# Optimization experiments

Hardware: AMD Instinct MI355X
Metric: run time of the kernel (lower is better)

The kernel has to match this reference:

```python
import jax, jax.numpy as jnp
import numpy as np

EPS = 1e-12  # F.normalize eps

def _l2norm(v, axis):
    n = jnp.sqrt(jnp.sum(v * v, axis=axis, keepdims=True))
    return v / jnp.maximum(n, EPS)

def setup_inputs() -> dict:
    key = jax.random.key(0)
    k1, k2, k3, k4 = jax.random.split(key, 4)
    B, N, D, K = 32, 8192, 128, 64
    x = jax.random.normal(k1, (B, N, D), dtype=jnp.float32)
    centroids = jnp.clip(0.01 * jax.random.normal(k2, (K, D), dtype=jnp.float32), -2.0, 2.0)
    conv_w = jax.random.normal(k3, (K, D), dtype=jnp.float32) / np.sqrt(D)
    conv_b = jax.random.normal(k4, (K,), dtype=jnp.float32) * 0.01
    return {"x": x, "centroids": centroids, "conv_w": conv_w, "conv_b": conv_b}

def reference(x, centroids, conv_w, conv_b):
    B, N, D = x.shape
    K = centroids.shape[0]
    # normalize_input: L2 over descriptor dim
    xn = _l2norm(x, axis=2)                                   # [B,N,D]
    # 1x1 conv == linear projection, softmax over clusters
    logits = jnp.einsum('bnd,kd->bnk', xn, conv_w) + conv_b   # [B,N,K]
    a = jax.nn.softmax(logits, axis=2)                        # [B,N,K]
    # vlad_{bkd} = sum_n a_{bnk} (x_{bnd} - c_{kd})
    #           = (a^T x)_{bkd} - c_{kd} * sum_n a_{bnk}
    ax = jnp.einsum('bnk,bnd->bkd', a, xn)                    # [B,K,D]
    a_sum = jnp.sum(a, axis=1)                                # [B,K]
    vlad = ax - centroids[None, :, :] * a_sum[:, :, None]     # [B,K,D]
    # intra-normalize, flatten, global normalize
    vlad = _l2norm(vlad, axis=2)
    vlad = vlad.reshape(B, K * D)
    vlad = _l2norm(vlad, axis=1)
    return vlad
```

## Files before the change

### kernel.cpp

```cpp
#include <hip/hip_runtime.h>
#include <hip/hip_bf16.h>
#include <math.h>

namespace {

typedef float f32x4 __attribute__((ext_vector_type(4)));
typedef float f32x16 __attribute__((ext_vector_type(16)));
typedef short bf16x8 __attribute__((ext_vector_type(8)));

constexpr int Bc = 32, Nc = 8192, Dc = 128, Kc = 64;
constexpr int PB = 32;
constexpr int RPB = Nc / PB;
constexpr int NT = 64;
constexpr int ITERS = RPB / NT;
constexpr int XSTR = 136;

__device__ __forceinline__ unsigned int pk(float a, float b) {
  union { __hip_bfloat162 h; unsigned int u; } c;
  c.h = __float22bfloat162_rn(make_float2(a, b));
  return c.u;
}
__device__ __forceinline__ unsigned short f2b(float f) {
  union { __hip_bfloat16 h; unsigned short u; } c;
  c.h = __float2bfloat16(f);
  return c.u;
}
__device__ __forceinline__ float b2f(unsigned short u) {
  union { unsigned int i; float f; } c;
  c.i = ((unsigned int)u) << 16;
  return c.f;
}

__global__ __launch_bounds__(256) void nv_k1(
    const float* __restrict__ x, const float* __restrict__ conv_w,
    const float* __restrict__ conv_b, float* __restrict__ accP,
    float* __restrict__ asumP) {
  __shared__ __align__(16) short xS[NT * XSTR];
  __shared__ __align__(16) short aT[Kc * NT];

  const int tid = threadIdx.x;
  const int w = tid >> 6, l = tid & 63;
  const int bp = blockIdx.x;
  const int b = bp / PB, p = bp % PB;
  const float* xb = x + (size_t)b * Nc * Dc + (size_t)p * RPB * Dc;

  bf16x8 wf[4][4];
#pragma unroll
  for (int nt = 0; nt < 4; ++nt) {
    const int k = (l & 15) + 16 * nt;
#pragma unroll
    for (int ks = 0; ks < 4; ++ks) {
      const float* wp = conv_w + k * Dc + 8 * (l >> 4) + 32 * ks;
      const float4 w0 = *(const float4*)wp;
      const float4 w1 = *(const float4*)(wp + 4);
      union { unsigned int u[4]; bf16x8 v; } fu;
      fu.u[0] = pk(w0.x, w0.y); fu.u[1] = pk(w0.z, w0.w);
      fu.u[2] = pk(w1.x, w1.y); fu.u[3] = pk(w1.z, w1.w);
      wf[nt][ks] = fu.v;
    }
  }
  float cb16[4][4];
#pragma unroll
  for (int nt = 0; nt < 4; ++nt)
#pragma unroll
    for (int i = 0; i < 4; ++i)
      cb16[nt][i] = conv_b[16 * nt + 4 * (l >> 4) + i];

  f32x16 acc2[2];
#pragma unroll
  for (int mt = 0; mt < 2; ++mt)
#pragma unroll
    for (int r = 0; r < 16; ++r) acc2[mt][r] = 0.f;
  float asum_acc = 0.f;

  const int sr = tid >> 2, sq = tid & 3;
  float4 cur[8];
  {
    const float* gp = xb + (size_t)sr * Dc + 32 * sq;
#pragma unroll
    for (int j = 0; j < 8; ++j) cur[j] = *(const float4*)(gp + 4 * j);
  }

  const int dcol = (l & 31) + 32 * w;
  const int nmy = 16 * w + (l & 15);

  for (int it = 0; it < ITERS; ++it) {
    float ss = 0.f;
#pragma unroll
    for (int j = 0; j < 8; ++j)
      ss += cur[j].x * cur[j].x + cur[j].y * cur[j].y +
            cur[j].z * cur[j].z + cur[j].w * cur[j].w;
    ss += __shfl_xor(ss, 1);
    ss += __shfl_xor(ss, 2);
    const float invn = 1.0f / fmaxf(sqrtf(ss), 1e-12f);
    unsigned int xv[16];
#pragma unroll
    for (int j = 0; j < 8; ++j) {
      xv[2 * j] = pk(cur[j].x * invn, cur[j].y * invn);
      xv[2 * j + 1] = pk(cur[j].z * invn, cur[j].w * invn);
    }
    __syncthreads();
    {
      short* dst = xS + sr * XSTR + 32 * sq;
#pragma unroll
      for (int j = 0; j < 4; ++j) {
        union { unsigned int u[4]; bf16x8 v; } fu;
        fu.u[0] = xv[4 * j]; fu.u[1] = xv[4 * j + 1];
        fu.u[2] = xv[4 * j + 2]; fu.u[3] = xv[4 * j + 3];
        *(bf16x8*)(dst + 8 * j) = fu.v;
      }
    }
    float4 nxt[8];
    if (it + 1 < ITERS) {
      const float* gp = xb + (size_t)((it + 1) * NT + sr) * Dc + 32 * sq;
#pragma unroll
      for (int j = 0; j < 8; ++j) nxt[j] = *(const float4*)(gp + 4 * j);
    }
    __syncthreads();

    f32x4 c1[4];
#pragma unroll
    for (int nt = 0; nt < 4; ++nt) {
      c1[nt][0] = 0.f; c1[nt][1] = 0.f; c1[nt][2] = 0.f; c1[nt][3] = 0.f;
    }
#pragma unroll
    for (int ks = 0; ks < 4; ++ks) {
      const bf16x8 af =
          *(const bf16x8*)(xS + (16 * w + (l & 15)) * XSTR + 8 * (l >> 4) + 32 * ks);
#pragma unroll
      for (int nt = 0; nt < 4; ++nt)
        c1[nt] = __builtin_amdgcn_mfma_f32_16x16x32_bf16(wf[nt][ks], af,
                                                         c1[nt], 0, 0, 0);
    }

    float e[4][4];
    float s = 0.f;
#pragma unroll
    for (int nt = 0; nt < 4; ++nt)
#pragma unroll
      for (int i = 0; i < 4; ++i) {
        e[nt][i] = __expf(c1[nt][i] + cb16[nt][i]);
        s += e[nt][i];
      }
    s += __shfl_xor(s, 16);
    s += __shfl_xor(s, 32);
    const float inv = __builtin_amdgcn_rcpf(s);

    {
      const int cn = nmy >> 2, nb = nmy & 3;
#pragma unroll
      for (int nt = 0; nt < 4; ++nt)
#pragma unroll
        for (int i = 0; i < 4; ++i) {
          const int k = 16 * nt + 4 * (l >> 4) + i;
          aT[k * NT + ((cn ^ (k & 15)) << 2) + nb] = (short)f2b(e[nt][i] * inv);
        }
    }
    __syncthreads();

    {
      const short* rp = aT + (tid >> 2) * NT + (tid & 3) * 16;
      union { uint4 q; unsigned short h[8]; } q0, q1;
      q0.q = *(const uint4*)rp;
      q1.q = *(const uint4*)(rp + 8);
      float ps = 0.f;
#pragma unroll
      for (int j = 0; j < 8; ++j) ps += b2f(q0.h[j]) + b2f(q1.h[j]);
      ps += __shfl_xor(ps, 1);
      ps += __shfl_xor(ps, 2);
      asum_acc += ps;
    }

#pragma unroll
    for (int ks2 = 0; ks2 < 4; ++ks2) {
      const int n0 = 16 * ks2 + 8 * (l >> 5);
      union { unsigned int u[4]; bf16x8 v; } bu;
#pragma unroll
      for (int j = 0; j < 4; ++j) {
        const unsigned short s0 =
            *(const unsigned short*)(xS + (n0 + 2 * j) * XSTR + dcol);
        const unsigned short s1 =
            *(const unsigned short*)(xS + (n0 + 2 * j + 1) * XSTR + dcol);
        bu.u[j] = (unsigned int)s0 | ((unsigned int)s1 << 16);
      }
#pragma unroll
      for (int mt = 0; mt < 2; ++mt) {
        const int k = (l & 31) + 32 * mt;
        const int cn = n0 >> 2;
        const uint2 lo = *(const uint2*)(aT + k * NT + (((cn)     ^ (k & 15)) << 2));
        const uint2 hi = *(const uint2*)(aT + k * NT + (((cn + 1) ^ (k & 15)) << 2));
        union { unsigned int u[4]; bf16x8 v; } au;
        au.u[0] = lo.x; au.u[1] = lo.y; au.u[2] = hi.x; au.u[3] = hi.y;
        acc2[mt] = __builtin_amdgcn_mfma_f32_32x32x16_bf16(au.v, bu.v,
                                                           acc2[mt], 0, 0, 0);
      }
    }
#pragma unroll
    for (int j = 0; j < 8; ++j) cur[j] = nxt[j];
  }

  if ((tid & 3) == 0) asumP[(size_t)bp * Kc + (tid >> 2)] = asum_acc;
  float* ap = accP + (size_t)bp * (Kc * Dc);
#pragma unroll
  for (int mt = 0; mt < 2; ++mt)
#pragma unroll
    for (int r = 0; r < 16; ++r) {
      const int k = 32 * mt + (r & 3) + 8 * (r >> 2) + 4 * (l >> 5);
      ap[k * Dc + dcol] = acc2[mt][r];
    }
}

__global__ __launch_bounds__(64) void nv_k2(
    const float* __restrict__ accP, const float* __restrict__ asumP,
    const float* __restrict__ cent, float* __restrict__ out,
    float* __restrict__ gssK) {
  const int t = threadIdx.x;
  const int b = blockIdx.x >> 6;
  const int k = blockIdx.x & 63;

  float av = 0.f;
  if (t >= 32) av = asumP[(size_t)(b * PB + (t - 32)) * Kc + k];
  av += __shfl_xor(av, 1);
  av += __shfl_xor(av, 2);
  av += __shfl_xor(av, 4);
  av += __shfl_xor(av, 8);
  av += __shfl_xor(av, 16);
  const float as = __shfl(av, 32);

  float v0 = 0.f, v1 = 0.f;
#pragma unroll
  for (int pp = 0; pp < PB; ++pp) {
    const float2 tt = *(const float2*)(accP + (size_t)(b * PB + pp) * (Kc * Dc) +
                                       k * Dc + 2 * t);
    v0 += tt.x;
    v1 += tt.y;
  }
  const float2 c2 = *(const float2*)(cent + (size_t)k * Dc + 2 * t);
  v0 -= c2.x * as;
  v1 -= c2.y * as;
  float ssk = v0 * v0 + v1 * v1;
#pragma unroll
  for (int o = 1; o < 64; o <<= 1) ssk += __shfl_xor(ssk, o);
  const float sc = 1.0f / fmaxf(sqrtf(ssk), 1e-12f);
  float2* o2 = reinterpret_cast<float2*>(out + (size_t)b * (Kc * Dc) + k * Dc + 2 * t);
  *o2 = make_float2(v0 * sc, v1 * sc);
  if (t == 0) gssK[(size_t)b * Kc + k] = ssk * sc * sc;
}

__global__ __launch_bounds__(256) void nv_k3(float* __restrict__ out,
                                             const float* __restrict__ gssK) {
  const int bid = blockIdx.x;
  const int b = bid >> 3;
  float g = 0.f;
#pragma unroll
  for (int i = 0; i < 64; ++i) g += gssK[(size_t)b * Kc + i];
  const float gsc = 1.0f / fmaxf(sqrtf(g), 1e-12f);
  float4* o4 = reinterpret_cast<float4*>(out) + (size_t)bid * 256 + threadIdx.x;
  float4 v = *o4;
  v.x *= gsc;
  v.y *= gsc;
  v.z *= gsc;
  v.w *= gsc;
  *o4 = v;
}

}

extern "C" void kernel_launch(void* const* d_in, const int* in_sizes, int n_in,
                              void* d_out, int out_size, void* d_ws,
                              size_t ws_size, hipStream_t stream) {
  const float* x = (const float*)d_in[0];
  const float* ce = (const float*)d_in[1];
  const float* cw = (const float*)d_in[2];
  const float* cb = (const float*)d_in[3];
  float* out = (float*)d_out;

  const size_t accPf = (size_t)Bc * PB * Kc * Dc;
  const size_t asumPf = (size_t)Bc * PB * Kc;
  float* accP = (float*)d_ws;
  float* asumP = accP + accPf;
  float* gssK = asumP + asumPf;

  nv_k1<<<Bc * PB, 256, 0, stream>>>(x, cw, cb, accP, asumP);
  nv_k2<<<Bc * Kc, 64, 0, stream>>>(accP, asumP, ce, out, gssK);
  nv_k3<<<Bc * 8, 256, 0, stream>>>(out, gssK);
}
```

Measured before the change: 65.57 us.

## Double-buffer LDS tiles to drop a barrier and regroup reduction kernel into 256-thread blocks

The main kernel now alternates between two LDS buffers for the normalized x tile and the softmax weights, so the barrier before the next tile is written can be removed. This cuts one __syncthreads per iteration at the cost of doubled shared memory. The partial-sum kernel is reorganized so each 256-thread block handles 8 clusters, with a cooperative asum reduction and per-block global-norm partials, which reduces the final kernel's reads. Fewer, larger blocks in the second kernel may lower parallelism for the bandwidth-bound partial reduction.

Result: slower. 71.67 us (+9.3%).

```diff
diff --git a/kernel.cpp b/kernel.cpp
--- a/kernel.cpp
+++ b/kernel.cpp
@@ -35,8 +35,8 @@
     const float* __restrict__ x, const float* __restrict__ conv_w,
     const float* __restrict__ conv_b, float* __restrict__ accP,
     float* __restrict__ asumP) {
-  __shared__ __align__(16) short xS[NT * XSTR];
-  __shared__ __align__(16) short aT[Kc * NT];
+  __shared__ __align__(16) short xS[2][NT * XSTR];
+  __shared__ __align__(16) short aT[2][Kc * NT];
 
   const int tid = threadIdx.x;
   const int w = tid >> 6, l = tid & 63;
@@ -85,6 +85,10 @@
   const int nmy = 16 * w + (l & 15);
 
   for (int it = 0; it < ITERS; ++it) {
+    const int c = it & 1;
+    short* xSc = &xS[c][0];
+    short* aTc = &aT[c][0];
+
     float ss = 0.f;
 #pragma unroll
     for (int j = 0; j < 8; ++j)
@@ -93,20 +97,15 @@
     ss += __shfl_xor(ss, 1);
     ss += __shfl_xor(ss, 2);
     const float invn = 1.0f / fmaxf(sqrtf(ss), 1e-12f);
-    unsigned int xv[16];
-#pragma unroll
-    for (int j = 0; j < 8; ++j) {
-      xv[2 * j] = pk(cur[j].x * invn, cur[j].y * invn);
-      xv[2 * j + 1] = pk(cur[j].z * invn, cur[j].w * invn);
-    }
-    __syncthreads();
     {
-      short* dst = xS + sr * XSTR + 32 * sq;
+      short* dst = xSc + sr * XSTR + 32 * sq;
 #pragma unroll
       for (int j = 0; j < 4; ++j) {
         union { unsigned int u[4]; bf16x8 v; } fu;
-        fu.u[0] = xv[4 * j]; fu.u[1] = xv[4 * j + 1];
-        fu.u[2] = xv[4 * j + 2]; fu.u[3] = xv[4 * j + 3];
+        fu.u[0] = pk(cur[2 * j].x * invn, cur[2 * j].y * invn);
+        fu.u[1] = pk(cur[2 * j].z * invn, cur[2 * j].w * invn);
+        fu.u[2] = pk(cur[2 * j + 1].x * invn, cur[2 * j + 1].y * invn);
+        fu.u[3] = pk(cur[2 * j + 1].z * invn, cur[2 * j + 1].w * invn);
         *(bf16x8*)(dst + 8 * j) = fu.v;
       }
     }
@@ -126,7 +125,7 @@
 #pragma unroll
     for (int ks = 0; ks < 4; ++ks) {
       const bf16x8 af =
-          *(const bf16x8*)(xS + (16 * w + (l & 15)) * XSTR + 8 * (l >> 4) + 32 * ks);
+          *(const bf16x8*)(xSc + (16 * w + (l & 15)) * XSTR + 8 * (l >> 4) + 32 * ks);
 #pragma unroll
       for (int nt = 0; nt < 4; ++nt)
         c1[nt] = __builtin_amdgcn_mfma_f32_16x16x32_bf16(wf[nt][ks], af,
@@ -153,13 +152,13 @@
 #pragma unroll
         for (int i = 0; i < 4; ++i) {
           const int k = 16 * nt + 4 * (l >> 4) + i;
-          aT[k * NT + ((cn ^ (k & 15)) << 2) + nb] = (short)f2b(e[nt][i] * inv);
+          aTc[k * NT + ((cn ^ (k & 15)) << 2) + nb] = (short)f2b(e[nt][i] * inv);
         }
     }
     __syncthreads();
 
     {
-      const short* rp = aT + (tid >> 2) * NT + (tid & 3) * 16;
+      const short* rp = aTc + (tid >> 2) * NT + (tid & 3) * 16;
       union { uint4 q; unsigned short h[8]; } q0, q1;
       q0.q = *(const uint4*)rp;
       q1.q = *(const uint4*)(rp + 8);
@@ -178,25 +177,27 @@
 #pragma unroll
       for (int j = 0; j < 4; ++j) {
         const unsigned short s0 =
-            *(const unsigned short*)(xS + (n0 + 2 * j) * XSTR + dcol);
+            *(const unsigned short*)(xSc + (n0 + 2 * j) * XSTR + dcol);
         const unsigned short s1 =
-            *(const unsigned short*)(xS + (n0 + 2 * j + 1) * XSTR + dcol);
+            *(const unsigned short*)(xSc + (n0 + 2 * j + 1) * XSTR + dcol);
         bu.u[j] = (unsigned int)s0 | ((unsigned int)s1 << 16);
       }
 #pragma unroll
       for (int mt = 0; mt < 2; ++mt) {
         const int k = (l & 31) + 32 * mt;
         const int cn = n0 >> 2;
-        const uint2 lo = *(const uint2*)(aT + k * NT + (((cn)     ^ (k & 15)) << 2));
-        const uint2 hi = *(const uint2*)(aT + k * NT + (((cn + 1) ^ (k & 15)) << 2));
+        const uint2 lo = *(const uint2*)(aTc + k * NT + (((cn)     ^ (k & 15)) << 2));
+        const uint2 hi = *(const uint2*)(aTc + k * NT + (((cn + 1) ^ (k & 15)) << 2));
         union { unsigned int u[4]; bf16x8 v; } au;
         au.u[0] = lo.x; au.u[1] = lo.y; au.u[2] = hi.x; au.u[3] = hi.y;
         acc2[mt] = __builtin_amdgcn_mfma_f32_32x32x16_bf16(au.v, bu.v,
                                                            acc2[mt], 0, 0, 0);
       }
     }
-#pragma unroll
-    for (int j = 0; j < 8; ++j) cur[j] = nxt[j];
+    if (it + 1 < ITERS) {
+#pragma unroll
+      for (int j = 0; j < 8; ++j) cur[j] = nxt[j];
+    }
   }
 
   if ((tid & 3) == 0) asumP[(size_t)bp * Kc + (tid >> 2)] = asum_acc;
@@ -210,50 +211,67 @@
     }
 }
 
-__global__ __launch_bounds__(64) void nv_k2(
+__global__ __launch_bounds__(256) void nv_k2(
     const float* __restrict__ accP, const float* __restrict__ asumP,
     const float* __restrict__ cent, float* __restrict__ out,
-    float* __restrict__ gssK) {
-  const int t = threadIdx.x;
-  const int b = blockIdx.x >> 6;
-  const int k = blockIdx.x & 63;
-
-  float av = 0.f;
-  if (t >= 32) av = asumP[(size_t)(b * PB + (t - 32)) * Kc + k];
-  av += __shfl_xor(av, 1);
-  av += __shfl_xor(av, 2);
-  av += __shfl_xor(av, 4);
-  av += __shfl_xor(av, 8);
-  av += __shfl_xor(av, 16);
-  const float as = __shfl(av, 32);
-
-  float v0 = 0.f, v1 = 0.f;
-#pragma unroll
-  for (int pp = 0; pp < PB; ++pp) {
-    const float2 tt = *(const float2*)(accP + (size_t)(b * PB + pp) * (Kc * Dc) +
-                                       k * Dc + 2 * t);
-    v0 += tt.x;
-    v1 += tt.y;
-  }
-  const float2 c2 = *(const float2*)(cent + (size_t)k * Dc + 2 * t);
-  v0 -= c2.x * as;
-  v1 -= c2.y * as;
-  float ssk = v0 * v0 + v1 * v1;
-#pragma unroll
-  for (int o = 1; o < 64; o <<= 1) ssk += __shfl_xor(ssk, o);
-  const float sc = 1.0f / fmaxf(sqrtf(ssk), 1e-12f);
-  float2* o2 = reinterpret_cast<float2*>(out + (size_t)b * (Kc * Dc) + k * Dc + 2 * t);
-  *o2 = make_float2(v0 * sc, v1 * sc);
-  if (t == 0) gssK[(size_t)b * Kc + k] = ssk * sc * sc;
+    float* __restrict__ gssP) {
+  __shared__ float asumS[8];
+  __shared__ float redS[8][33];
+  __shared__ float gssWv[4];
+  const int tid = threadIdx.x;
+  const int w = tid >> 6, l = tid & 63;
+  const int b = blockIdx.x >> 3;
+  const int kg = blockIdx.x & 7;
+
+  {
+    const int kk = tid >> 5, pp = tid & 31;
+    redS[kk][pp] = asumP[(size_t)(b * PB + pp) * Kc + kg * 8 + kk];
+  }
+  __syncthreads();
+  if (tid < 8) {
+    float s = 0.f;
+#pragma unroll
+    for (int q = 0; q < 32; ++q) s += redS[tid][q];
+    asumS[tid] = s;
+  }
+  __syncthreads();
+
+  float gss = 0.f;
+#pragma unroll
+  for (int ki = 0; ki < 2; ++ki) {
+    const int kloc = w + 4 * ki, k = kg * 8 + kloc;
+    float v0 = 0.f, v1 = 0.f;
+    for (int pp = 0; pp < PB; ++pp) {
+      const float2 t = *(const float2*)(accP + (size_t)(b * PB + pp) * (Kc * Dc) +
+                                        k * Dc + 2 * l);
+      v0 += t.x;
+      v1 += t.y;
+    }
+    const float as = asumS[kloc];
+    const float2 c2 = *(const float2*)(cent + (size_t)k * Dc + 2 * l);
+    v0 -= c2.x * as;
+    v1 -= c2.y * as;
+    float ssk = v0 * v0 + v1 * v1;
+#pragma unroll
+    for (int o = 1; o < 64; o <<= 1) ssk += __shfl_xor(ssk, o);
+    const float sc = 1.0f / fmaxf(sqrtf(ssk), 1e-12f);
+    gss += ssk * sc * sc;
+    float2* o2 =
+        reinterpret_cast<float2*>(out + (size_t)b * (Kc * Dc) + k * Dc + 2 * l);
+    *o2 = make_float2(v0 * sc, v1 * sc);
+  }
+  if (l == 0) gssWv[w] = gss;
+  __syncthreads();
+  if (tid == 0) gssP[blockIdx.x] = gssWv[0] + gssWv[1] + gssWv[2] + gssWv[3];
 }
 
 __global__ __launch_bounds__(256) void nv_k3(float* __restrict__ out,
-                                             const float* __restrict__ gssK) {
+                                             const float* __restrict__ gssP) {
   const int bid = blockIdx.x;
   const int b = bid >> 3;
   float g = 0.f;
 #pragma unroll
-  for (int i = 0; i < 64; ++i) g += gssK[(size_t)b * Kc + i];
+  for (int i = 0; i < 8; ++i) g += gssP[b * 8 + i];
   const float gsc = 1.0f / fmaxf(sqrtf(g), 1e-12f);
   float4* o4 = reinterpret_cast<float4*>(out) + (size_t)bid * 256 + threadIdx.x;
   float4 v = *o4;
@@ -279,9 +297,9 @@
   const size_t asumPf = (size_t)Bc * PB * Kc;
   float* accP = (float*)d_ws;
   float* asumP = accP + accPf;
-  float* gssK = asumP + asumPf;
+  float* gssP = asumP + asumPf;
 
   nv_k1<<<Bc * PB, 256, 0, stream>>>(x, cw, cb, accP, asumP);
-  nv_k2<<<Bc * Kc, 64, 0, stream>>>(accP, asumP, ce, out, gssK);
-  nv_k3<<<Bc * 8, 256, 0, stream>>>(out, gssK);
-}
+  nv_k2<<<Bc * 8, 256, 0, stream>>>(accP, asumP, ce, out, gssP);
+  nv_k3<<<Bc * 8, 256, 0, stream>>>(out, gssP);
+}
```
